# Kernel tuning notes

Measured on AMD Instinct MI355X. Metric: run time of the kernel, lower is better.

The kernel has to match this reference:

```python
import math
import jax, jax.numpy as jnp
import numpy as np

# Frozen random shifts from the original module's __init__ (random.randint(-1,1))
SHIFT_C = 1   # p_2_0_1: roll along channel dim
SHIFT_H = 1   # p_4_1_0: roll along h
SHIFT_W = -1  # p_4_1_1: roll along w
K = 7         # horizontal window size (F.unfold kernel (1,7), padding (0,3))


def setup_inputs() -> dict:
    key = jax.random.key(0)
    k1, k2 = jax.random.split(key)
    n, c, h, w = 8, 256, 56, 56
    x = jax.random.normal(k1, (n, c, h, w), dtype=jnp.float32)
    # p_1_w ~ trunc_normal(std=0.1) around 1.0; approximate with 1 + 0.1*normal
    p1w = 1.0 + 0.1 * jax.random.normal(k2, (1, c, h, w), dtype=jnp.float32)
    return {"x": x, "p1w": p1w}


def _unfold_w7(t):
    # t: (n,c,h,w) -> (n,c,7,h,w): 7 horizontal taps, zero-padded (pad=3)
    w = t.shape[-1]
    tp = jnp.pad(t, ((0, 0), (0, 0), (0, 0), (3, 3)))
    return jnp.stack([tp[..., j:j + w] for j in range(K)], axis=2)


def reference(x, p1w):
    n, c, h, w = x.shape
    hw = h * w
    t1 = p1w * x                              # (n,c,h,w)
    t2 = jnp.roll(t1, SHIFT_C, axis=1)        # roll channels
    t3 = _unfold_w7(t2)                       # (n,c,7,h,w)
    t4 = jnp.roll(jnp.roll(t3, SHIFT_H, axis=3), SHIFT_W, axis=4)
    t5 = t1[:, :, None] - t3                  # (n,c,7,h,w)
    t6 = x[:, :, None] + t4                   # (n,c,7,h,w)
    x2 = x.reshape(n, c, hw)
    t5r = t5.reshape(n, c, K, hw)
    t6r = t6.reshape(n, c, K, hw)
    # scores: bmm(x (n,c,hw), t5^T (n,hw,c*7)) -> (n,c,c,7)
    t7 = jnp.einsum('nip,njkp->nijk', x2, t5r) / math.sqrt(hw)
    # aggregate: bmm(t7 (n,c,c*7), t6 (n,c*7,hw)) -> (n,c,hw)
    t8 = jnp.einsum('nijk,njkp->nip', t7, t6r) / math.sqrt(c * K)
    return t8.reshape(n, c, h, w)
```

## Files before the change

kernel.cpp:

```cpp
#include <hip/hip_runtime.h>

typedef unsigned short u16;
typedef __bf16 bf16x8 __attribute__((ext_vector_type(8)));
typedef float f32x4 __attribute__((ext_vector_type(4)));

#define HH  56
#define WW  56
#define HW  3136
#define CC  256
#define NB  8
#define CKP 2048
#define KS1 4

__device__ __forceinline__ u16 f2bf(float f) {
  unsigned int u = __float_as_uint(f);
  u += 0x7fffu + ((u >> 16) & 1u);
  return (u16)(u >> 16);
}
__device__ __forceinline__ float bf2f(u16 v) {
  return __uint_as_float((unsigned)v << 16);
}

__device__ __forceinline__ void lds_load16(const void* g, void* l) {
  __builtin_amdgcn_global_load_lds(
      (const __attribute__((address_space(1))) void*)g,
      (__attribute__((address_space(3))) void*)l, 16, 0, 0);
}

__global__ void pass1(const float* __restrict__ x, const float* __restrict__ p1w,
                      u16* __restrict__ t1b, u16* __restrict__ xb) {
  int i = blockIdx.x * 256 + threadIdx.x;
  int cw = i % (CC * HW / 4);
  float4 xv = ((const float4*)x)[i];
  float4 wv = ((const float4*)p1w)[cw];
  uint2 xo = make_uint2((unsigned)f2bf(xv.x) | ((unsigned)f2bf(xv.y) << 16),
                        (unsigned)f2bf(xv.z) | ((unsigned)f2bf(xv.w) << 16));
  ((uint2*)xb)[i] = xo;
  uint2 to = make_uint2((unsigned)f2bf(xv.x * wv.x) | ((unsigned)f2bf(xv.y * wv.y) << 16),
                        (unsigned)f2bf(xv.z * wv.z) | ((unsigned)f2bf(xv.w * wv.w) << 16));
  ((uint2*)t1b)[i] = to;
}

__global__ __launch_bounds__(256)
void gemm1f(const u16* __restrict__ A, const u16* __restrict__ t1b,
            float* __restrict__ Cp) {
  __shared__ u16 As[128 * 64];
  __shared__ u16 Bs[128 * 64];

  const int z = blockIdx.z, nb = z / KS1, ks = z % KS1;
  const int it0 = 49 * ks / KS1, it1 = 49 * (ks + 1) / KS1;
  const u16* Ab  = A   + (long)nb * CC * HW;
  const u16* t1n = t1b + (long)nb * CC * HW;
  const int m0 = blockIdx.x * 128, n0 = blockIdx.y * 128;
  const int jb = blockIdx.y * 16;
  const int t = threadIdx.x;
  const int lane = t & 63, wave = t >> 6;
  const int wm = wave & 1, wn = wave >> 1;
  const int lm = lane & 15, quad = lane >> 4;

  const int jl = (t >> 3) & 15, pc = t & 7, hf = t >> 7;
  const int j  = jb + jl;
  const int jm = (j + CC - 1) & (CC - 1);
  const u16* arow = t1n + (long)j  * HW;
  const u16* wrow = t1n + (long)jm * HW;

  f32x4 acc[4][4];
#pragma unroll
  for (int a = 0; a < 4; ++a)
#pragma unroll
    for (int b = 0; b < 4; ++b) acc[a][b] = (f32x4)0.0f;

  int rowc[4], colc[4];
#pragma unroll
  for (int ci = 0; ci < 4; ++ci) {
    int c = t + ci * 256;
    rowc[ci] = c >> 3;
    colc[ci] = ((c & 7) ^ (rowc[ci] & 7)) * 8;
  }

  for (int it = it0; it < it1; ++it) {
    const int k0 = it * 64;
#pragma unroll
    for (int ci = 0; ci < 4; ++ci)
      lds_load16(Ab + (long)(m0 + rowc[ci]) * HW + k0 + colc[ci],
                 &As[(t + ci * 256) * 8]);

    {
      const int p8 = k0 + pc * 8;
      __attribute__((aligned(16))) u16 Ar[8];
      __attribute__((aligned(16))) u16 Wd[24];
      *(uint4*)Ar = *(const uint4*)&arow[p8];
#pragma unroll
      for (int L = 0; L < 3; ++L) {
        int ad = p8 - 8 + L * 8;
        ad = ad < 0 ? 0 : (ad > HW - 8 ? HW - 8 : ad);
        *(uint4*)&Wd[L * 8] = *(const uint4*)&wrow[ad];
      }
      const int w0t = p8 % 56;
      int wv[8];
#pragma unroll
      for (int e = 0; e < 8; ++e) { int w = w0t + e; wv[e] = w >= 56 ? w - 56 : w; }
      if (hf == 0) {
#pragma unroll
        for (int k = 0; k < 4; ++k) {
          __attribute__((aligned(16))) u16 v[8];
#pragma unroll
          for (int e = 0; e < 8; ++e)
            v[e] = ((unsigned)(wv[e] + k - 3) < 56u) ? Wd[e + k + 5] : (u16)0;
          *(uint4*)&Bs[(jl * 8 + k) * 64 + (pc ^ k) * 8] = *(const uint4*)v;
        }
      } else {
#pragma unroll
        for (int k = 4; k < 7; ++k) {
          __attribute__((aligned(16))) u16 v[8];
#pragma unroll
          for (int e = 0; e < 8; ++e)
            v[e] = ((unsigned)(wv[e] + k - 3) < 56u) ? Wd[e + k + 5] : (u16)0;
          *(uint4*)&Bs[(jl * 8 + k) * 64 + (pc ^ k) * 8] = *(const uint4*)v;
        }
        *(uint4*)&Bs[(jl * 8 + 7) * 64 + (pc ^ 7) * 8] = *(const uint4*)Ar;
      }
    }
    __syncthreads();
#pragma unroll
    for (int kk = 0; kk < 2; ++kk) {
      const int phys = ((kk * 4 + quad) ^ (lm & 7)) * 8;
      bf16x8 af[4], bv[4];
#pragma unroll
      for (int mi = 0; mi < 4; ++mi)
        af[mi] = *(const bf16x8*)&As[(wm * 64 + mi * 16 + lm) * 64 + phys];
#pragma unroll
      for (int ni = 0; ni < 4; ++ni)
        bv[ni] = *(const bf16x8*)&Bs[(wn * 64 + ni * 16 + lm) * 64 + phys];
#pragma unroll
      for (int mi = 0; mi < 4; ++mi)
#pragma unroll
        for (int ni = 0; ni < 4; ++ni)
          acc[mi][ni] = __builtin_amdgcn_mfma_f32_16x16x32_bf16(
              af[mi], bv[ni], acc[mi][ni], 0, 0, 0);
    }
    __syncthreads();
  }

  float* Cb = Cp + ((long)ks * NB + nb) * (long)CC * CKP;
#pragma unroll
  for (int mi = 0; mi < 4; ++mi)
#pragma unroll
    for (int ni = 0; ni < 4; ++ni) {
      int rb = m0 + wm * 64 + mi * 16 + quad * 4;
      int cg = n0 + wn * 64 + ni * 16 + lm;
#pragma unroll
      for (int r = 0; r < 4; ++r)
        Cb[(long)(rb + r) * CKP + cg] = acc[mi][ni][r];
    }
}

__global__ void reduce1(const float* __restrict__ p1, u16* __restrict__ t7) {
  const int g = blockIdx.x * 256 + threadIdx.x;
  const long S = (long)NB * CC * CKP;
  const long base = (long)g * 8;
  float a[8];
#pragma unroll
  for (int e = 0; e < 8; ++e) a[e] = 0.0f;
#pragma unroll
  for (int ks = 0; ks < KS1; ++ks) {
    float4 lo = *(const float4*)&p1[ks * S + base];
    float4 hi = *(const float4*)&p1[ks * S + base + 4];
    a[0] += lo.x; a[1] += lo.y; a[2] += lo.z; a[3] += lo.w;
    a[4] += hi.x; a[5] += hi.y; a[6] += hi.z; a[7] += hi.w;
  }
  const float s = 1.0f / 56.0f;
  const float G = a[7];
  __attribute__((aligned(16))) u16 o[8];
  float s7 = 0.0f;
#pragma unroll
  for (int k = 0; k < 7; ++k) {
    float v = (G - a[k]) * s;
    s7 += v;
    o[k] = f2bf(v);
  }
  o[7] = f2bf(s7);
  *(uint4*)&t7[base] = *(const uint4*)o;
}

__global__ __launch_bounds__(256)
void gemm2f(const u16* __restrict__ A, const u16* __restrict__ xb,
            const u16* __restrict__ t1b, float* __restrict__ out) {
  __shared__ u16 As[128 * 64];
  __shared__ u16 Bs[64 * 64];

  const int nb = blockIdx.z;
  const u16* Ab  = A   + (long)nb * CC * CKP;
  const u16* xbn = xb  + (long)nb * CC * HW;
  const u16* t1n = t1b + (long)nb * CC * HW;
  const int m0 = blockIdx.x * 128, n0 = blockIdx.y * 64;
  const int t = threadIdx.x;
  const int lane = t & 63, wave = t >> 6;
  const int wm = wave & 1, wn = wave >> 1;
  const int lm = lane & 15, quad = lane >> 4;

  const int pr = t & 63, jg = t >> 6;
  const int p  = n0 + pr;
  const int h  = p / WW, w = p - h * WW;
  const int h2 = (h + HH - 1) % HH;
  const int w2 = (w + 1) % WW;
  const int swz = pr & 7;

  int toff[7], tmsk[7];
#pragma unroll
  for (int k = 0; k < 7; ++k) {
    int ww = w2 + k - 3;
    int wc = ww < 0 ? 0 : (ww > 55 ? 55 : ww);
    toff[k] = h2 * WW + wc;
    tmsk[k] = ((unsigned)ww < 56u);
  }

  f32x4 acc[4][2];
#pragma unroll
  for (int a = 0; a < 4; ++a)
#pragma unroll
    for (int b = 0; b < 2; ++b) acc[a][b] = (f32x4)0.0f;

  int rowc[4], colc[4];
#pragma unroll
  for (int ci = 0; ci < 4; ++ci) {
    int c = t + ci * 256;
    rowc[ci] = c >> 3;
    colc[ci] = ((c & 7) ^ (rowc[ci] & 7)) * 8;
  }

  u16 tr[2][7], xr[2];
#pragma unroll
  for (int jj = 0; jj < 2; ++jj) {
    const int jch = jg * 2 + jj;
    const int jmm = (jch + CC - 1) & (CC - 1);
    const u16* trow = t1n + (long)jmm * HW;
#pragma unroll
    for (int k = 0; k < 7; ++k) tr[jj][k] = trow[toff[k]];
    xr[jj] = xbn[(long)jch * HW + p];
  }

  for (int it = 0; it < 32; ++it) {
    const int k0 = it * 64;
#pragma unroll
    for (int ci = 0; ci < 4; ++ci)
      lds_load16(Ab + (long)(m0 + rowc[ci]) * CKP + k0 + colc[ci],
                 &As[(t + ci * 256) * 8]);

#pragma unroll
    for (int jj = 0; jj < 2; ++jj) {
      __attribute__((aligned(16))) u16 v[8];
#pragma unroll
      for (int k = 0; k < 7; ++k) v[k] = tmsk[k] ? tr[jj][k] : (u16)0;
      v[7] = xr[jj];
      *(uint4*)&Bs[pr * 64 + (((jg * 2 + jj) ^ swz) * 8)] = *(const uint4*)v;
    }
    __syncthreads();

    if (it < 31) {
#pragma unroll
      for (int jj = 0; jj < 2; ++jj) {
        const int jch = (it + 1) * 8 + jg * 2 + jj;
        const int jmm = (jch + CC - 1) & (CC - 1);
        const u16* trow = t1n + (long)jmm * HW;
#pragma unroll
        for (int k = 0; k < 7; ++k) tr[jj][k] = trow[toff[k]];
        xr[jj] = xbn[(long)jch * HW + p];
      }
    }

#pragma unroll
    for (int kk = 0; kk < 2; ++kk) {
      const int phys = ((kk * 4 + quad) ^ (lm & 7)) * 8;
      bf16x8 af[4], bv[2];
#pragma unroll
      for (int mi = 0; mi < 4; ++mi)
        af[mi] = *(const bf16x8*)&As[(wm * 64 + mi * 16 + lm) * 64 + phys];
#pragma unroll
      for (int ni = 0; ni < 2; ++ni)
        bv[ni] = *(const bf16x8*)&Bs[(wn * 32 + ni * 16 + lm) * 64 + phys];
#pragma unroll
      for (int mi = 0; mi < 4; ++mi)
#pragma unroll
        for (int ni = 0; ni < 2; ++ni)
          acc[mi][ni] = __builtin_amdgcn_mfma_f32_16x16x32_bf16(
              af[mi], bv[ni], acc[mi][ni], 0, 0, 0);
    }
    __syncthreads();
  }

  const float s2 = 0.023622783f;
  float* Ob = out + (long)nb * CC * HW;
#pragma unroll
  for (int mi = 0; mi < 4; ++mi)
#pragma unroll
    for (int ni = 0; ni < 2; ++ni) {
      int rb = m0 + wm * 64 + mi * 16 + quad * 4;
      int cg = n0 + wn * 32 + ni * 16 + lm;
#pragma unroll
      for (int r = 0; r < 4; ++r)
        Ob[(long)(rb + r) * HW + cg] = acc[mi][ni][r] * s2;
    }
}

extern "C" void kernel_launch(void* const* d_in, const int* in_sizes, int n_in,
                              void* d_out, int out_size, void* d_ws, size_t ws_size,
                              hipStream_t stream) {
  const float* x   = (const float*)d_in[0];
  const float* p1w = (const float*)d_in[1];

  char* ws = (char*)d_ws;
  size_t o = 0;
  u16* xb  = (u16*)(ws + o); o += (size_t)NB * CC * HW * 2;
  u16* t1b = (u16*)(ws + o); o += (size_t)NB * CC * HW * 2;
  u16* t7  = (u16*)(ws + o); o += (size_t)NB * CC * CKP * 2;
  float* p1 = (float*)(ws + o); o += (size_t)KS1 * NB * CC * CKP * 4;

  pass1<<<NB * CC * HW / 4 / 256, 256, 0, stream>>>(x, p1w, t1b, xb);
  gemm1f<<<dim3(2, 16, NB * KS1), 256, 0, stream>>>(xb, t1b, p1);
  reduce1<<<NB * CC * CKP / 8 / 256, 256, 0, stream>>>(p1, t7);
  gemm2f<<<dim3(2, 49, NB), 256, 0, stream>>>(t7, xb, t1b, (float*)d_out);
}
```

Measured before the change: 210.8 us.

## Double-buffer LDS tiles in both GEMM kernels to overlap loads with MFMA

Both GEMM kernels now use ping-pong shared-memory buffers for A and B tiles. The async global-to-LDS copy and the B-tile construction for the next k-step are issued before the MFMA work on the current step, with register prefetch one step further ahead. This hides global load latency behind compute and halves the barriers per tile. In exchange, LDS use per block doubles (64KB in gemm1f), which may lower occupancy, and register pressure rises from the extra prefetch buffers.

Result: slower. 223.5 us (+6.0%).

```diff
diff --git a/kernel.cpp b/kernel.cpp
--- a/kernel.cpp
+++ b/kernel.cpp
@@ -44,11 +44,12 @@
 __global__ __launch_bounds__(256)
 void gemm1f(const u16* __restrict__ A, const u16* __restrict__ t1b,
             float* __restrict__ Cp) {
-  __shared__ u16 As[128 * 64];
-  __shared__ u16 Bs[128 * 64];
+  __shared__ u16 As0[128 * 64], As1[128 * 64];
+  __shared__ u16 Bs0[128 * 64], Bs1[128 * 64];
 
   const int z = blockIdx.z, nb = z / KS1, ks = z % KS1;
   const int it0 = 49 * ks / KS1, it1 = 49 * (ks + 1) / KS1;
+  const int nIt = it1 - it0;
   const u16* Ab  = A   + (long)nb * CC * HW;
   const u16* t1n = t1b + (long)nb * CC * HW;
   const int m0 = blockIdx.x * 128, n0 = blockIdx.y * 128;
@@ -78,69 +79,98 @@
     colc[ci] = ((c & 7) ^ (rowc[ci] & 7)) * 8;
   }
 
-  for (int it = it0; it < it1; ++it) {
-    const int k0 = it * 64;
-#pragma unroll
-    for (int ci = 0; ci < 4; ++ci)
-      lds_load16(Ab + (long)(m0 + rowc[ci]) * HW + k0 + colc[ci],
-                 &As[(t + ci * 256) * 8]);
-
-    {
-      const int p8 = k0 + pc * 8;
-      __attribute__((aligned(16))) u16 Ar[8];
-      __attribute__((aligned(16))) u16 Wd[24];
-      *(uint4*)Ar = *(const uint4*)&arow[p8];
-#pragma unroll
-      for (int L = 0; L < 3; ++L) {
-        int ad = p8 - 8 + L * 8;
-        ad = ad < 0 ? 0 : (ad > HW - 8 ? HW - 8 : ad);
-        *(uint4*)&Wd[L * 8] = *(const uint4*)&wrow[ad];
-      }
-      const int w0t = p8 % 56;
-      int wv[8];
-#pragma unroll
-      for (int e = 0; e < 8; ++e) { int w = w0t + e; wv[e] = w >= 56 ? w - 56 : w; }
-      if (hf == 0) {
-#pragma unroll
-        for (int k = 0; k < 4; ++k) {
-          __attribute__((aligned(16))) u16 v[8];
-#pragma unroll
-          for (int e = 0; e < 8; ++e)
-            v[e] = ((unsigned)(wv[e] + k - 3) < 56u) ? Wd[e + k + 5] : (u16)0;
-          *(uint4*)&Bs[(jl * 8 + k) * 64 + (pc ^ k) * 8] = *(const uint4*)v;
-        }
-      } else {
-#pragma unroll
-        for (int k = 4; k < 7; ++k) {
-          __attribute__((aligned(16))) u16 v[8];
-#pragma unroll
-          for (int e = 0; e < 8; ++e)
-            v[e] = ((unsigned)(wv[e] + k - 3) < 56u) ? Wd[e + k + 5] : (u16)0;
-          *(uint4*)&Bs[(jl * 8 + k) * 64 + (pc ^ k) * 8] = *(const uint4*)v;
-        }
-        *(uint4*)&Bs[(jl * 8 + 7) * 64 + (pc ^ 7) * 8] = *(const uint4*)Ar;
-      }
+  __attribute__((aligned(16))) u16 ArE[8], ArO[8];
+  __attribute__((aligned(16))) u16 WdE[24], WdO[24];
+
+#define DMA1(AsD, itn) do { const int k0_ = (itn) * 64;                        \
+    _Pragma("unroll")                                                          \
+    for (int ci = 0; ci < 4; ++ci)                                             \
+      lds_load16(Ab + (long)(m0 + rowc[ci]) * HW + k0_ + colc[ci],             \
+                 &AsD[(t + ci * 256) * 8]); } while (0)
+
+#define PF1(Ar, Wd, itn) do { const int p8_ = (itn) * 64 + pc * 8;             \
+    *(uint4*)(Ar) = *(const uint4*)&arow[p8_];                                 \
+    _Pragma("unroll")                                                          \
+    for (int L = 0; L < 3; ++L) {                                              \
+      int ad = p8_ - 8 + L * 8;                                                \
+      ad = ad < 0 ? 0 : (ad > HW - 8 ? HW - 8 : ad);                           \
+      *(uint4*)&(Wd)[L * 8] = *(const uint4*)&wrow[ad]; } } while (0)
+
+#define BUILD1(Ar, Wd, BsD, itn) do {                                          \
+    const int p8_ = (itn) * 64 + pc * 8;                                       \
+    const int w0t_ = p8_ % 56;                                                 \
+    int wvx_[8];                                                               \
+    _Pragma("unroll")                                                          \
+    for (int e = 0; e < 8; ++e) { int wq = w0t_ + e;                           \
+      wvx_[e] = wq >= 56 ? wq - 56 : wq; }                                     \
+    if (hf == 0) {                                                             \
+      _Pragma("unroll")                                                        \
+      for (int k = 0; k < 4; ++k) {                                            \
+        __attribute__((aligned(16))) u16 v_[8];                                \
+        _Pragma("unroll")                                                      \
+        for (int e = 0; e < 8; ++e)                                            \
+          v_[e] = ((unsigned)(wvx_[e] + k - 3) < 56u) ? (Wd)[e + k + 5] : (u16)0; \
+        *(uint4*)&(BsD)[(jl * 8 + k) * 64 + (pc ^ k) * 8] = *(const uint4*)v_; \
+      }                                                                        \
+    } else {                                                                   \
+      _Pragma("unroll")                                                        \
+      for (int k = 4; k < 7; ++k) {                                            \
+        __attribute__((aligned(16))) u16 v_[8];                                \
+        _Pragma("unroll")                                                      \
+        for (int e = 0; e < 8; ++e)                                            \
+          v_[e] = ((unsigned)(wvx_[e] + k - 3) < 56u) ? (Wd)[e + k + 5] : (u16)0; \
+        *(uint4*)&(BsD)[(jl * 8 + k) * 64 + (pc ^ k) * 8] = *(const uint4*)v_; \
+      }                                                                        \
+      *(uint4*)&(BsD)[(jl * 8 + 7) * 64 + (pc ^ 7) * 8] = *(const uint4*)(Ar); \
+    } } while (0)
+
+#define MF1(AsS, BsS) do {                                                     \
+    _Pragma("unroll")                                                          \
+    for (int kk = 0; kk < 2; ++kk) {                                           \
+      const int phys = ((kk * 4 + quad) ^ (lm & 7)) * 8;                       \
+      bf16x8 af[4], bv[4];                                                     \
+      _Pragma("unroll")                                                        \
+      for (int mi = 0; mi < 4; ++mi)                                           \
+        af[mi] = *(const bf16x8*)&(AsS)[(wm * 64 + mi * 16 + lm) * 64 + phys]; \
+      _Pragma("unroll")                                                        \
+      for (int ni = 0; ni < 4; ++ni)                                           \
+        bv[ni] = *(const bf16x8*)&(BsS)[(wn * 64 + ni * 16 + lm) * 64 + phys]; \
+      _Pragma("unroll")                                                        \
+      for (int mi = 0; mi < 4; ++mi)                                           \
+        _Pragma("unroll")                                                      \
+        for (int ni = 0; ni < 4; ++ni)                                         \
+          acc[mi][ni] = __builtin_amdgcn_mfma_f32_16x16x32_bf16(               \
+              af[mi], bv[ni], acc[mi][ni], 0, 0, 0);                           \
+    } } while (0)
+
+  PF1(ArE, WdE, it0);
+  DMA1(As0, it0);
+  BUILD1(ArE, WdE, Bs0, it0);
+  PF1(ArO, WdO, it0 + 1);
+  __syncthreads();
+
+  for (int il = 0; il + 2 <= nIt; il += 2) {
+    DMA1(As1, it0 + il + 1);
+    BUILD1(ArO, WdO, Bs1, it0 + il + 1);
+    if (il + 2 < nIt) PF1(ArE, WdE, it0 + il + 2);
+    MF1(As0, Bs0);
+    __syncthreads();
+    if (il + 2 < nIt) {
+      DMA1(As0, it0 + il + 2);
+      BUILD1(ArE, WdE, Bs0, it0 + il + 2);
+      if (il + 3 < nIt) PF1(ArO, WdO, it0 + il + 3);
     }
+    MF1(As1, Bs1);
     __syncthreads();
-#pragma unroll
-    for (int kk = 0; kk < 2; ++kk) {
-      const int phys = ((kk * 4 + quad) ^ (lm & 7)) * 8;
-      bf16x8 af[4], bv[4];
-#pragma unroll
-      for (int mi = 0; mi < 4; ++mi)
-        af[mi] = *(const bf16x8*)&As[(wm * 64 + mi * 16 + lm) * 64 + phys];
-#pragma unroll
-      for (int ni = 0; ni < 4; ++ni)
-        bv[ni] = *(const bf16x8*)&Bs[(wn * 64 + ni * 16 + lm) * 64 + phys];
-#pragma unroll
-      for (int mi = 0; mi < 4; ++mi)
-#pragma unroll
-        for (int ni = 0; ni < 4; ++ni)
-          acc[mi][ni] = __builtin_amdgcn_mfma_f32_16x16x32_bf16(
-              af[mi], bv[ni], acc[mi][ni], 0, 0, 0);
-    }
-    __syncthreads();
-  }
+  }
+  if (nIt & 1) {
+    MF1(As0, Bs0);
+  }
+
+#undef DMA1
+#undef PF1
+#undef BUILD1
+#undef MF1
 
   float* Cb = Cp + ((long)ks * NB + nb) * (long)CC * CKP;
 #pragma unroll
@@ -186,8 +216,8 @@
 __global__ __launch_bounds__(256)
 void gemm2f(const u16* __restrict__ A, const u16* __restrict__ xb,
             const u16* __restrict__ t1b, float* __restrict__ out) {
-  __shared__ u16 As[128 * 64];
-  __shared__ u16 Bs[64 * 64];
+  __shared__ u16 As0[128 * 64], As1[128 * 64];
+  __shared__ u16 Bs0[64 * 64], Bs1[64 * 64];
 
   const int nb = blockIdx.z;
   const u16* Ab  = A   + (long)nb * CC * CKP;
@@ -229,65 +259,79 @@
     colc[ci] = ((c & 7) ^ (rowc[ci] & 7)) * 8;
   }
 
-  u16 tr[2][7], xr[2];
-#pragma unroll
-  for (int jj = 0; jj < 2; ++jj) {
-    const int jch = jg * 2 + jj;
-    const int jmm = (jch + CC - 1) & (CC - 1);
-    const u16* trow = t1n + (long)jmm * HW;
-#pragma unroll
-    for (int k = 0; k < 7; ++k) tr[jj][k] = trow[toff[k]];
-    xr[jj] = xbn[(long)jch * HW + p];
-  }
-
-  for (int it = 0; it < 32; ++it) {
-    const int k0 = it * 64;
-#pragma unroll
-    for (int ci = 0; ci < 4; ++ci)
-      lds_load16(Ab + (long)(m0 + rowc[ci]) * CKP + k0 + colc[ci],
-                 &As[(t + ci * 256) * 8]);
-
-#pragma unroll
-    for (int jj = 0; jj < 2; ++jj) {
-      __attribute__((aligned(16))) u16 v[8];
-#pragma unroll
-      for (int k = 0; k < 7; ++k) v[k] = tmsk[k] ? tr[jj][k] : (u16)0;
-      v[7] = xr[jj];
-      *(uint4*)&Bs[pr * 64 + (((jg * 2 + jj) ^ swz) * 8)] = *(const uint4*)v;
+  u16 trE[2][7], xrE[2], trO[2][7], xrO[2];
+
+#define DMA2(AsD, itn) do { const int k0_ = (itn) * 64;                        \
+    _Pragma("unroll")                                                          \
+    for (int ci = 0; ci < 4; ++ci)                                             \
+      lds_load16(Ab + (long)(m0 + rowc[ci]) * CKP + k0_ + colc[ci],            \
+                 &AsD[(t + ci * 256) * 8]); } while (0)
+
+#define PF2(tr, xr, itn) do {                                                  \
+    _Pragma("unroll")                                                          \
+    for (int jj = 0; jj < 2; ++jj) {                                           \
+      const int jch = (itn) * 8 + jg * 2 + jj;                                 \
+      const int jmm = (jch + CC - 1) & (CC - 1);                               \
+      const u16* trow = t1n + (long)jmm * HW;                                  \
+      _Pragma("unroll")                                                        \
+      for (int k = 0; k < 7; ++k) (tr)[jj][k] = trow[toff[k]];                 \
+      (xr)[jj] = xbn[(long)jch * HW + p]; } } while (0)
+
+#define BUILD2(tr, xr, BsD) do {                                               \
+    _Pragma("unroll")                                                          \
+    for (int jj = 0; jj < 2; ++jj) {                                           \
+      __attribute__((aligned(16))) u16 v_[8];                                  \
+      _Pragma("unroll")                                                        \
+      for (int k = 0; k < 7; ++k) v_[k] = tmsk[k] ? (tr)[jj][k] : (u16)0;      \
+      v_[7] = (xr)[jj];                                                        \
+      *(uint4*)&(BsD)[pr * 64 + (((jg * 2 + jj) ^ swz) * 8)] =                 \
+          *(const uint4*)v_; } } while (0)
+
+#define MF2(AsS, BsS) do {                                                     \
+    _Pragma("unroll")                                                          \
+    for (int kk = 0; kk < 2; ++kk) {                                           \
+      const int phys = ((kk * 4 + quad) ^ (lm & 7)) * 8;                       \
+      bf16x8 af[4], bv[2];                                                     \
+      _Pragma("unroll")                                                        \
+      for (int mi = 0; mi < 4; ++mi)                                           \
+        af[mi] = *(const bf16x8*)&(AsS)[(wm * 64 + mi * 16 + lm) * 64 + phys]; \
+      _Pragma("unroll")                                                        \
+      for (int ni = 0; ni < 2; ++ni)                                           \
+        bv[ni] = *(const bf16x8*)&(BsS)[(wn * 32 + ni * 16 + lm) * 64 + phys]; \
+      _Pragma("unroll")                                                        \
+      for (int mi = 0; mi < 4; ++mi)                                           \
+        _Pragma("unroll")                                                      \
+        for (int ni = 0; ni < 2; ++ni)                                         \
+          acc[mi][ni] = __builtin_amdgcn_mfma_f32_16x16x32_bf16(               \
+              af[mi], bv[ni], acc[mi][ni], 0, 0, 0);                           \
+    } } while (0)
+
+  PF2(trE, xrE, 0);
+  DMA2(As0, 0);
+  BUILD2(trE, xrE, Bs0);
+  PF2(trO, xrO, 1);
+  __syncthreads();
+
+  for (int itp = 0; itp < 16; ++itp) {
+    const int itE = itp * 2;
+    DMA2(As1, itE + 1);
+    BUILD2(trO, xrO, Bs1);
+    if (itE + 2 < 32) PF2(trE, xrE, itE + 2);
+    MF2(As0, Bs0);
+    __syncthreads();
+    if (itE + 2 < 32) {
+      DMA2(As0, itE + 2);
+      BUILD2(trE, xrE, Bs0);
+      if (itE + 3 < 32) PF2(trO, xrO, itE + 3);
     }
+    MF2(As1, Bs1);
     __syncthreads();
-
-    if (it < 31) {
-#pragma unroll
-      for (int jj = 0; jj < 2; ++jj) {
-        const int jch = (it + 1) * 8 + jg * 2 + jj;
-        const int jmm = (jch + CC - 1) & (CC - 1);
-        const u16* trow = t1n + (long)jmm * HW;
-#pragma unroll
-        for (int k = 0; k < 7; ++k) tr[jj][k] = trow[toff[k]];
-        xr[jj] = xbn[(long)jch * HW + p];
-      }
-    }
-
-#pragma unroll
-    for (int kk = 0; kk < 2; ++kk) {
-      const int phys = ((kk * 4 + quad) ^ (lm & 7)) * 8;
-      bf16x8 af[4], bv[2];
-#pragma unroll
-      for (int mi = 0; mi < 4; ++mi)
-        af[mi] = *(const bf16x8*)&As[(wm * 64 + mi * 16 + lm) * 64 + phys];
-#pragma unroll
-      for (int ni = 0; ni < 2; ++ni)
-        bv[ni] = *(const bf16x8*)&Bs[(wn * 32 + ni * 16 + lm) * 64 + phys];
-#pragma unroll
-      for (int mi = 0; mi < 4; ++mi)
-#pragma unroll
-        for (int ni = 0; ni < 2; ++ni)
-          acc[mi][ni] = __builtin_amdgcn_mfma_f32_16x16x32_bf16(
-              af[mi], bv[ni], acc[mi][ni], 0, 0, 0);
-    }
-    __syncthreads();
-  }
+  }
+
+#undef DMA2
+#undef PF2
+#undef BUILD2
+#undef MF2
 
   const float s2 = 0.023622783f;
   float* Ob = out + (long)nb * CC * HW;
```

## Flatten GEMM grids with batch-fastest block order and drop gemm2 B register prefetch

Applied to the files above, without the earlier changes.

Both GEMM kernels now launch a 1D grid and decode the block index so the batch index varies fastest. Consecutive blocks therefore land on different batches, which changes how work spreads across the XCDs and their L2 caches. In gemm2f, the register prefetch of the next iteration's gathered t1/x values is removed; they are now loaded directly right before the LDS store. This lowers register pressure but exposes the gather latency before each sync.

New measurement: 185.6 us. 1.14x faster.

```diff
diff --git a/kernel.cpp b/kernel.cpp
--- a/kernel.cpp
+++ b/kernel.cpp
@@ -47,12 +47,19 @@
   __shared__ u16 As[128 * 64];
   __shared__ u16 Bs[128 * 64];
 
-  const int z = blockIdx.z, nb = z / KS1, ks = z % KS1;
+  const int bi = blockIdx.x;
+  const int nb = bi & 7;
+  const int r  = bi >> 3;
+  const int ks = r & 3;
+  const int r2 = r >> 2;
+  const int m0b = r2 & 1;
+  const int n0b = r2 >> 1;
+
   const int it0 = 49 * ks / KS1, it1 = 49 * (ks + 1) / KS1;
   const u16* Ab  = A   + (long)nb * CC * HW;
   const u16* t1n = t1b + (long)nb * CC * HW;
-  const int m0 = blockIdx.x * 128, n0 = blockIdx.y * 128;
-  const int jb = blockIdx.y * 16;
+  const int m0 = m0b * 128, n0 = n0b * 128;
+  const int jb = n0b * 16;
   const int t = threadIdx.x;
   const int lane = t & 63, wave = t >> 6;
   const int wm = wave & 1, wn = wave >> 1;
@@ -150,8 +157,8 @@
       int rb = m0 + wm * 64 + mi * 16 + quad * 4;
       int cg = n0 + wn * 64 + ni * 16 + lm;
 #pragma unroll
-      for (int r = 0; r < 4; ++r)
-        Cb[(long)(rb + r) * CKP + cg] = acc[mi][ni][r];
+      for (int r4 = 0; r4 < 4; ++r4)
+        Cb[(long)(rb + r4) * CKP + cg] = acc[mi][ni][r4];
     }
 }
 
@@ -189,11 +196,16 @@
   __shared__ u16 As[128 * 64];
   __shared__ u16 Bs[64 * 64];
 
-  const int nb = blockIdx.z;
+  const int bi = blockIdx.x;
+  const int nb = bi & 7;
+  const int r  = bi >> 3;
+  const int m0b = r & 1;
+  const int n0b = r >> 1;
+
   const u16* Ab  = A   + (long)nb * CC * CKP;
   const u16* xbn = xb  + (long)nb * CC * HW;
   const u16* t1n = t1b + (long)nb * CC * HW;
-  const int m0 = blockIdx.x * 128, n0 = blockIdx.y * 64;
+  const int m0 = m0b * 128, n0 = n0b * 64;
   const int t = threadIdx.x;
   const int lane = t & 63, wave = t >> 6;
   const int wm = wave & 1, wn = wave >> 1;
@@ -229,17 +241,6 @@
     colc[ci] = ((c & 7) ^ (rowc[ci] & 7)) * 8;
   }
 
-  u16 tr[2][7], xr[2];
-#pragma unroll
-  for (int jj = 0; jj < 2; ++jj) {
-    const int jch = jg * 2 + jj;
-    const int jmm = (jch + CC - 1) & (CC - 1);
-    const u16* trow = t1n + (long)jmm * HW;
-#pragma unroll
-    for (int k = 0; k < 7; ++k) tr[jj][k] = trow[toff[k]];
-    xr[jj] = xbn[(long)jch * HW + p];
-  }
-
   for (int it = 0; it < 32; ++it) {
     const int k0 = it * 64;
 #pragma unroll
@@ -249,26 +250,19 @@
 
 #pragma unroll
     for (int jj = 0; jj < 2; ++jj) {
+      const int jch = it * 8 + jg * 2 + jj;
+      const int jmm = (jch + CC - 1) & (CC - 1);
+      const u16* trow = t1n + (long)jmm * HW;
       __attribute__((aligned(16))) u16 v[8];
 #pragma unroll
-      for (int k = 0; k < 7; ++k) v[k] = tmsk[k] ? tr[jj][k] : (u16)0;
-      v[7] = xr[jj];
+      for (int k = 0; k < 7; ++k) {
+        u16 tv = trow[toff[k]];
+        v[k] = tmsk[k] ? tv : (u16)0;
+      }
+      v[7] = xbn[(long)jch * HW + p];
       *(uint4*)&Bs[pr * 64 + (((jg * 2 + jj) ^ swz) * 8)] = *(const uint4*)v;
     }
     __syncthreads();
-
-    if (it < 31) {
-#pragma unroll
-      for (int jj = 0; jj < 2; ++jj) {
-        const int jch = (it + 1) * 8 + jg * 2 + jj;
-        const int jmm = (jch + CC - 1) & (CC - 1);
-        const u16* trow = t1n + (long)jmm * HW;
-#pragma unroll
-        for (int k = 0; k < 7; ++k) tr[jj][k] = trow[toff[k]];
-        xr[jj] = xbn[(long)jch * HW + p];
-      }
-    }
-
 #pragma unroll
     for (int kk = 0; kk < 2; ++kk) {
       const int phys = ((kk * 4 + quad) ^ (lm & 7)) * 8;
@@ -298,8 +292,8 @@
       int rb = m0 + wm * 64 + mi * 16 + quad * 4;
       int cg = n0 + wn * 32 + ni * 16 + lm;
 #pragma unroll
-      for (int r = 0; r < 4; ++r)
-        Ob[(long)(rb + r) * HW + cg] = acc[mi][ni][r] * s2;
+      for (int r4 = 0; r4 < 4; ++r4)
+        Ob[(long)(rb + r4) * HW + cg] = acc[mi][ni][r4] * s2;
     }
 }
 
@@ -317,7 +311,7 @@
   float* p1 = (float*)(ws + o); o += (size_t)KS1 * NB * CC * CKP * 4;
 
   pass1<<<NB * CC * HW / 4 / 256, 256, 0, stream>>>(x, p1w, t1b, xb);
-  gemm1f<<<dim3(2, 16, NB * KS1), 256, 0, stream>>>(xb, t1b, p1);
+  gemm1f<<<NB * KS1 * 2 * 16, 256, 0, stream>>>(xb, t1b, p1);
   reduce1<<<NB * CC * CKP / 8 / 256, 256, 0, stream>>>(p1, t7);
-  gemm2f<<<dim3(2, 49, NB), 256, 0, stream>>>(t7, xb, t1b, (float*)d_out);
-}
+  gemm2f<<<NB * 2 * 49, 256, 0, stream>>>(t7, xb, t1b, (float*)d_out);
+}
```
